# Kernel tuning notes

Measured on AMD Instinct MI355X. Metric: run time of the kernel, lower is better.

Reference implementation:

```python
import jax, jax.numpy as jnp
import numpy as np

N_NODES = 1_000_000
N_EDGES = 16_000_000


def _lin_init(key, fan_in, fan_out):
    bound = 1.0 / np.sqrt(fan_in)
    kw, kb = jax.random.split(key)
    W = jax.random.uniform(kw, (fan_in, fan_out), jnp.float32, -bound, bound)
    b = jax.random.uniform(kb, (fan_out,), jnp.float32, -bound, bound)
    return W, b


def setup_inputs() -> dict:
    key = jax.random.key(0)
    ks = jax.random.split(key, 7)
    x = jax.random.normal(ks[0], (N_NODES, 2), jnp.float32)
    edge_index = jax.random.randint(ks[1], (2, N_EDGES), 0, N_NODES, dtype=jnp.int32)
    W1, b1 = _lin_init(ks[2], 2, 4)
    W2, b2 = _lin_init(ks[3], 4, 3)
    W3, b3 = _lin_init(ks[4], 3, 4)
    W4, b4 = _lin_init(ks[5], 4, 3)
    W5, b5 = _lin_init(ks[6], 3, 1)
    return {"x": x, "edge_index": edge_index,
            "W1": W1, "b1": b1, "W2": W2, "b2": b2,
            "W3": W3, "b3": b3, "W4": W4, "b4": b4,
            "W5": W5, "b5": b5}


def gcn_conv(x, W, b, src, dst, n):
    """PyG GCNConv: add self-loops, symmetric D^-1/2 (A+I) D^-1/2 normalization."""
    h = x @ W                                   # [n, out] transform first (tiny GEMM)
    loop = jnp.arange(n, dtype=src.dtype)
    s = jnp.concatenate([src, loop])            # sources incl. self loops
    d = jnp.concatenate([dst, loop])            # targets incl. self loops
    deg = jax.ops.segment_sum(jnp.ones(s.shape, h.dtype), d, num_segments=n)
    dinv = jnp.where(deg > 0, jax.lax.rsqrt(deg), 0.0)
    norm = dinv[s] * dinv[d]                    # [E+n]
    out = jax.ops.segment_sum(h[s] * norm[:, None], d, num_segments=n)
    return out + b


def reference(x, edge_index, W1, b1, W2, b2, W3, b3, W4, b4, W5, b5):
    n = x.shape[0]
    src, dst = edge_index[0], edge_index[1]
    h = jax.nn.relu(gcn_conv(x, W1, b1, src, dst, n))
    h = jax.nn.sigmoid(gcn_conv(h, W2, b2, src, dst, n))
    # saveLaplacianError only stores a scalar side-effect (self.llLoss); it does
    # not affect the returned output, so it is omitted.
    h = jax.nn.relu(h @ W3 + b3)
    h = jax.nn.relu(h @ W4 + b4)
    out = h @ W5 + b5                           # [n, 1]
    return jnp.squeeze(out, axis=-1)
```

## Files before the change

kernel.cpp:

```cpp
#include <hip/hip_runtime.h>
#include <hip/hip_bf16.h>
#include <hip/hip_fp16.h>


constexpr int NT = 256;
constexpr int SCAN_E = 1024;
constexpr int B2 = 11;
constexpr int BN = 1 << B2;
constexpr int NBMAX = 512;
constexpr int NBIN = 1024;
constexpr int TILE = 8192;
constexpr int AT = 1024;
constexpr int SENT = (int)0x80000000;

typedef int   v4i __attribute__((ext_vector_type(4)));
typedef float v2f __attribute__((ext_vector_type(2)));

__device__ __forceinline__ int4 ldnt4(const int* p) {
    v4i v = __builtin_nontemporal_load((const v4i*)p);
    int4 r; r.x = v.x; r.y = v.y; r.z = v.z; r.w = v.w; return r;
}
__device__ __forceinline__ float2 ldnt2f(const float* p) {
    v2f v = __builtin_nontemporal_load((const v2f*)p);
    return make_float2(v.x, v.y);
}
__device__ __forceinline__ float2 h2f2(unsigned u) {
    __half2 h = __builtin_bit_cast(__half2, u);
    return __half22float2(h);
}
__device__ __forceinline__ unsigned f2h2(float a, float b) {
    return __builtin_bit_cast(unsigned, __floats2half2_rn(a, b));
}
__device__ __forceinline__ void pk_add_lds(unsigned* p, unsigned v) {
    asm volatile("ds_pk_add_f16 %0, %1"
                 :: "v"((unsigned)(size_t)p), "v"(v) : "memory");
}

__global__ void k_binhist(const int* __restrict__ src, const int* __restrict__ dst,
                          int* __restrict__ ghist, int E, int halfN) {
    __shared__ int cnt[NBIN];
    int t0 = blockIdx.x * TILE;
    for (int l = threadIdx.x; l < NBIN; l += NT) cnt[l] = 0;
    __syncthreads();
    for (int k = 0; k < TILE / (NT * 4); ++k) {
        int idx = t0 + (k * NT + threadIdx.x) * 4;
        if (idx + 3 < E) {
            int4 d4 = ldnt4(dst + idx);
            int4 s4 = ldnt4(src + idx);
            atomicAdd(&cnt[((d4.x >> B2) << 1) | (s4.x >= halfN)], 1);
            atomicAdd(&cnt[((d4.y >> B2) << 1) | (s4.y >= halfN)], 1);
            atomicAdd(&cnt[((d4.z >> B2) << 1) | (s4.z >= halfN)], 1);
            atomicAdd(&cnt[((d4.w >> B2) << 1) | (s4.w >= halfN)], 1);
        } else {
            for (int j = 0; j < 4; ++j)
                if (idx + j < E) {
                    int s = src[idx + j], d = dst[idx + j];
                    atomicAdd(&cnt[((d >> B2) << 1) | (s >= halfN)], 1);
                }
        }
    }
    __syncthreads();
    for (int l = threadIdx.x; l < NBIN; l += NT)
        if (cnt[l]) atomicAdd(&ghist[l], cnt[l]);
}

__global__ void k_scanbuckets(const int* __restrict__ ghist, int* __restrict__ gbase,
                              int* __restrict__ gcur) {
    __shared__ int part[NBIN];
    int tid = threadIdx.x;
    int t = ghist[tid];
    int p = (t + 3) & ~3;
    part[tid] = p;
    __syncthreads();
    for (int off = 1; off < NBIN; off <<= 1) {
        int v = (tid >= off) ? part[tid - off] : 0;
        __syncthreads();
        part[tid] += v;
        __syncthreads();
    }
    int excl = part[tid] - p;
    gbase[tid] = excl; gcur[tid] = excl;
    if (tid == NBIN - 1) gbase[NBIN] = part[NBIN - 1];
}

__global__ void k_pad(const int* __restrict__ ghist, const int* __restrict__ gbase,
                      int* __restrict__ pairs) {
    int b = threadIdx.x;
    int e = gbase[b] + ghist[b];
    int nxt = gbase[b + 1];
    for (; e < nxt; ++e) pairs[e] = SENT;
}

__global__ void __launch_bounds__(512)
k_binscatter(const int* __restrict__ src, const int* __restrict__ dst,
             int* __restrict__ gcur, int* __restrict__ pairs,
             int E, int halfN) {
    __shared__ int cnt[NBIN], cur[NBIN], gpos[NBIN];
    __shared__ int lbase2[NBIN + 1];
    __shared__ int part[512];
    __shared__ int lbuf[TILE];
    __shared__ int totalSh;
    int t0 = blockIdx.x * TILE;
    int tid = threadIdx.x;
    cnt[2 * tid] = 0; cnt[2 * tid + 1] = 0;
    __syncthreads();
    for (int k = 0; k < TILE / (512 * 4); ++k) {
        int idx = t0 + (k * 512 + tid) * 4;
        if (idx + 3 < E) {
            int4 d4 = ldnt4(dst + idx);
            int4 s4 = ldnt4(src + idx);
            atomicAdd(&cnt[((d4.x >> B2) << 1) | (s4.x >= halfN)], 1);
            atomicAdd(&cnt[((d4.y >> B2) << 1) | (s4.y >= halfN)], 1);
            atomicAdd(&cnt[((d4.z >> B2) << 1) | (s4.z >= halfN)], 1);
            atomicAdd(&cnt[((d4.w >> B2) << 1) | (s4.w >= halfN)], 1);
        } else {
            for (int j = 0; j < 4; ++j)
                if (idx + j < E) {
                    int s = src[idx + j], d = dst[idx + j];
                    atomicAdd(&cnt[((d >> B2) << 1) | (s >= halfN)], 1);
                }
        }
    }
    __syncthreads();
    int c0 = cnt[2 * tid], c1 = cnt[2 * tid + 1];
    int t = c0 + c1;
    part[tid] = t;
    __syncthreads();
    for (int off = 1; off < 512; off <<= 1) {
        int v = (tid >= off) ? part[tid - off] : 0;
        __syncthreads();
        part[tid] += v;
        __syncthreads();
    }
    int ex = part[tid] - t;
    lbase2[2 * tid] = ex;          cur[2 * tid] = ex;
    lbase2[2 * tid + 1] = ex + c0; cur[2 * tid + 1] = ex + c0;
    if (tid == 511) { lbase2[NBIN] = part[511]; totalSh = part[511]; }
    if (c0) gpos[2 * tid]     = atomicAdd(&gcur[2 * tid], c0);
    if (c1) gpos[2 * tid + 1] = atomicAdd(&gcur[2 * tid + 1], c1);
    __syncthreads();
    for (int k = 0; k < TILE / (512 * 4); ++k) {
        int idx = t0 + (k * 512 + tid) * 4;
        if (idx + 3 < E) {
            int4 s4 = ldnt4(src + idx);
            int4 d4 = ldnt4(dst + idx);
            int b, sl;
            b = ((d4.x >> B2) << 1) | (s4.x >= halfN); sl = atomicAdd(&cur[b], 1);
            lbuf[sl] = s4.x | ((d4.x & (BN - 1)) << 20);
            b = ((d4.y >> B2) << 1) | (s4.y >= halfN); sl = atomicAdd(&cur[b], 1);
            lbuf[sl] = s4.y | ((d4.y & (BN - 1)) << 20);
            b = ((d4.z >> B2) << 1) | (s4.z >= halfN); sl = atomicAdd(&cur[b], 1);
            lbuf[sl] = s4.z | ((d4.z & (BN - 1)) << 20);
            b = ((d4.w >> B2) << 1) | (s4.w >= halfN); sl = atomicAdd(&cur[b], 1);
            lbuf[sl] = s4.w | ((d4.w & (BN - 1)) << 20);
        } else {
            for (int j = 0; j < 4; ++j) {
                if (idx + j < E) {
                    int s = src[idx + j], d = dst[idx + j];
                    int b = ((d >> B2) << 1) | (s >= halfN);
                    int sl = atomicAdd(&cur[b], 1);
                    lbuf[sl] = s | ((d & (BN - 1)) << 20);
                }
            }
        }
    }
    __syncthreads();
    int total = totalSh;
    for (int idx = tid; idx < total; idx += 512) {
        int lo = 0, hi = NBIN - 1;
        while (lo < hi) {
            int mid = (lo + hi + 1) >> 1;
            if (lbase2[mid] <= idx) lo = mid; else hi = mid - 1;
        }
        pairs[gpos[lo] + (idx - lbase2[lo])] = lbuf[idx];
    }
}

__global__ void __launch_bounds__(AT)
k_prep(const int* __restrict__ pairs, const int* __restrict__ gbase,
       const float2* __restrict__ x,
       float* __restrict__ dinv, unsigned* __restrict__ y16, int N) {
    __shared__ int cnt[BN];
    int b = blockIdx.x, tid = threadIdx.x;
    int eBeg = gbase[2 * b], eEnd = gbase[2 * b + 2];
    for (int l = tid; l < BN; l += AT) cnt[l] = 0;
    __syncthreads();
    for (int idx = eBeg + (tid << 2); idx < eEnd; idx += AT * 4) {
        int4 v4 = ldnt4(pairs + idx);
        atomicAdd(&cnt[(((unsigned)v4.x) >> 20) & (BN - 1)], (v4.x >= 0) ? 1 : 0);
        atomicAdd(&cnt[(((unsigned)v4.y) >> 20) & (BN - 1)], (v4.y >= 0) ? 1 : 0);
        atomicAdd(&cnt[(((unsigned)v4.z) >> 20) & (BN - 1)], (v4.z >= 0) ? 1 : 0);
        atomicAdd(&cnt[(((unsigned)v4.w) >> 20) & (BN - 1)], (v4.w >= 0) ? 1 : 0);
    }
    __syncthreads();
    int base = b << B2;
    for (int j = tid; j < BN; j += AT) {
        int i = base + j;
        if (i < N) {
            float di = rsqrtf((float)(cnt[j] + 1));
            dinv[i] = di;
            float2 xi = ldnt2f((const float*)(x + i));
            y16[i] = f2h2(xi.x * di, xi.y * di);
        }
    }
}

__global__ void __launch_bounds__(AT)
k_bagg1(const int* __restrict__ pairs, const int* __restrict__ gbase,
        const unsigned* __restrict__ y16, const float2* __restrict__ x,
        const float* __restrict__ dinv,
        const float* __restrict__ W1, const float* __restrict__ b1,
        const float* __restrict__ W2,
        float2* __restrict__ partA, float* __restrict__ partB,
        uint2* __restrict__ hfull, int N) {
    __shared__ unsigned accH[BN];
    int b = blockIdx.x, tid = threadIdx.x;
    int eBeg = gbase[2 * b], eEnd = gbase[2 * b + 2];
    for (int l = tid; l < BN; l += AT) accH[l] = 0u;
    __syncthreads();
    for (int idx = eBeg + (tid << 3); idx < eEnd; idx += AT * 8) {
        int4 a = ldnt4(pairs + idx);
        int idx2 = idx + 4;
        int4 bb;
        if (idx2 < eEnd) bb = ldnt4(pairs + idx2);
        else { bb.x = SENT; bb.y = SENT; bb.z = SENT; bb.w = SENT; }
        int sv[8] = {a.x, a.y, a.z, a.w, bb.x, bb.y, bb.z, bb.w};
        unsigned rv[8];
        #pragma unroll
        for (int q = 0; q < 8; ++q)
            rv[q] = y16[sv[q] & 0xFFFFF];
        #pragma unroll
        for (int q = 0; q < 8; ++q) {
            unsigned data = (sv[q] >= 0) ? rv[q] : 0u;
            int dl = (((unsigned)sv[q]) >> 20) & (BN - 1);
            pk_add_lds(&accH[dl], data);
        }
    }
    __syncthreads();
    int base = b << B2;
    for (int j = tid; j < BN; j += AT) {
        int i = base + j;
        if (i >= N) continue;
        float2 a = h2f2(accH[j]);
        float di = dinv[i];
        float2 xi = ldnt2f((const float*)(x + i));
        float ay0 = a.x + xi.x * di;
        float ay1 = a.y + xi.y * di;
        float o0 = fmaxf(di * (ay0 * W1[0] + ay1 * W1[4]) + b1[0], 0.f);
        float o1 = fmaxf(di * (ay0 * W1[1] + ay1 * W1[5]) + b1[1], 0.f);
        float o2 = fmaxf(di * (ay0 * W1[2] + ay1 * W1[6]) + b1[2], 0.f);
        float o3 = fmaxf(di * (ay0 * W1[3] + ay1 * W1[7]) + b1[3], 0.f);
        float h0 = (o0 * W2[0] + o1 * W2[3] + o2 * W2[6] + o3 * W2[9])  * di;
        float h1 = (o0 * W2[1] + o1 * W2[4] + o2 * W2[7] + o3 * W2[10]) * di;
        float hv2 = (o0 * W2[2] + o1 * W2[5] + o2 * W2[8] + o3 * W2[11]) * di;
        v2f sA; sA.x = h0; sA.y = h1;
        __builtin_nontemporal_store(sA, (v2f*)(partA + i));
        __builtin_nontemporal_store(hv2, partB + i);
        uint2 hp; hp.x = f2h2(h0, h1); hp.y = f2h2(hv2, 0.f);
        hfull[i] = hp;
    }
}

__global__ void __launch_bounds__(AT)
k_bagg2lo(const int* __restrict__ pairs, const int* __restrict__ gbase,
          const uint2* __restrict__ hfull,
          float2* __restrict__ partA, float* __restrict__ partB, int N) {
    __shared__ unsigned acc01[BN];
    __shared__ float acc2[BN];
    int b = blockIdx.x, tid = threadIdx.x;
    int eBeg = gbase[2 * b], eEnd = gbase[2 * b + 1];
    for (int l = tid; l < BN; l += AT) { acc01[l] = 0u; acc2[l] = 0.f; }
    __syncthreads();
    for (int idx = eBeg + (tid << 3); idx < eEnd; idx += AT * 8) {
        int4 a = ldnt4(pairs + idx);
        int idx2 = idx + 4;
        int4 bb;
        if (idx2 < eEnd) bb = ldnt4(pairs + idx2);
        else { bb.x = SENT; bb.y = SENT; bb.z = SENT; bb.w = SENT; }
        int sv[8] = {a.x, a.y, a.z, a.w, bb.x, bb.y, bb.z, bb.w};
        uint2 r[8];
        #pragma unroll
        for (int q = 0; q < 8; ++q)
            r[q] = hfull[sv[q] & 0xFFFFF];
        #pragma unroll
        for (int q = 0; q < 8; ++q) {
            int dl = (((unsigned)sv[q]) >> 20) & (BN - 1);
            unsigned d01 = (sv[q] >= 0) ? r[q].x : 0u;
            float    f2v = (sv[q] >= 0) ? h2f2(r[q].y).x : 0.f;
            pk_add_lds(&acc01[dl], d01);
            atomicAdd(&acc2[dl], f2v);
        }
    }
    __syncthreads();
    int base = b << B2;
    for (int j = tid; j < BN; j += AT) {
        int i = base + j;
        if (i >= N) continue;
        float2 a01 = h2f2(acc01[j]);
        float2 pa = ldnt2f((const float*)(partA + i));
        float pb = __builtin_nontemporal_load(partB + i);
        v2f oA; oA.x = pa.x + a01.x; oA.y = pa.y + a01.y;
        __builtin_nontemporal_store(oA, (v2f*)(partA + i));
        __builtin_nontemporal_store(pb + acc2[j], partB + i);
    }
}

__global__ void __launch_bounds__(AT)
k_bagg2hi(const int* __restrict__ pairs, const int* __restrict__ gbase,
          const uint2* __restrict__ hfull,
          const float2* __restrict__ partA, const float* __restrict__ partB,
          const float* __restrict__ dinv,
          const float* __restrict__ b2,
          const float* __restrict__ W3, const float* __restrict__ b3,
          const float* __restrict__ W4, const float* __restrict__ b4,
          const float* __restrict__ W5, const float* __restrict__ b5,
          float* __restrict__ out, int N) {
    __shared__ unsigned acc01[BN];
    __shared__ float acc2[BN];
    int b = blockIdx.x, tid = threadIdx.x;
    int eBeg = gbase[2 * b + 1], eEnd = gbase[2 * b + 2];
    for (int l = tid; l < BN; l += AT) { acc01[l] = 0u; acc2[l] = 0.f; }
    __syncthreads();
    for (int idx = eBeg + (tid << 3); idx < eEnd; idx += AT * 8) {
        int4 a = ldnt4(pairs + idx);
        int idx2 = idx + 4;
        int4 bb;
        if (idx2 < eEnd) bb = ldnt4(pairs + idx2);
        else { bb.x = SENT; bb.y = SENT; bb.z = SENT; bb.w = SENT; }
        int sv[8] = {a.x, a.y, a.z, a.w, bb.x, bb.y, bb.z, bb.w};
        uint2 r[8];
        #pragma unroll
        for (int q = 0; q < 8; ++q)
            r[q] = hfull[sv[q] & 0xFFFFF];
        #pragma unroll
        for (int q = 0; q < 8; ++q) {
            int dl = (((unsigned)sv[q]) >> 20) & (BN - 1);
            unsigned d01 = (sv[q] >= 0) ? r[q].x : 0u;
            float    f2v = (sv[q] >= 0) ? h2f2(r[q].y).x : 0.f;
            pk_add_lds(&acc01[dl], d01);
            atomicAdd(&acc2[dl], f2v);
        }
    }
    __syncthreads();
    int base = b << B2;
    for (int j = tid; j < BN; j += AT) {
        int i = base + j;
        if (i >= N) continue;
        float2 a01 = h2f2(acc01[j]);
        float2 pa = ldnt2f((const float*)(partA + i));
        float pb = __builtin_nontemporal_load(partB + i);
        float s0 = pa.x + a01.x;
        float s1 = pa.y + a01.y;
        float s2 = pb + acc2[j];
        float di = __builtin_nontemporal_load(dinv + i);
        float z0 = di * s0 + b2[0];
        float z1 = di * s1 + b2[1];
        float z2 = di * s2 + b2[2];
        float g0 = 1.f / (1.f + expf(-z0));
        float g1 = 1.f / (1.f + expf(-z1));
        float g2 = 1.f / (1.f + expf(-z2));
        float t0 = fmaxf(g0 * W3[0] + g1 * W3[4] + g2 * W3[8]  + b3[0], 0.f);
        float t1 = fmaxf(g0 * W3[1] + g1 * W3[5] + g2 * W3[9]  + b3[1], 0.f);
        float t2 = fmaxf(g0 * W3[2] + g1 * W3[6] + g2 * W3[10] + b3[2], 0.f);
        float t3 = fmaxf(g0 * W3[3] + g1 * W3[7] + g2 * W3[11] + b3[3], 0.f);
        float u0 = fmaxf(t0 * W4[0] + t1 * W4[3] + t2 * W4[6] + t3 * W4[9]  + b4[0], 0.f);
        float u1 = fmaxf(t0 * W4[1] + t1 * W4[4] + t2 * W4[7] + t3 * W4[10] + b4[1], 0.f);
        float u2 = fmaxf(t0 * W4[2] + t1 * W4[5] + t2 * W4[8] + t3 * W4[11] + b4[2], 0.f);
        out[i] = u0 * W5[0] + u1 * W5[1] + u2 * W5[2] + b5[0];
    }
}

__global__ void k_deg(const int* __restrict__ dst, int* __restrict__ deg, int E) {
    int e = blockIdx.x * blockDim.x + threadIdx.x;
    if (e < E) atomicAdd(deg + dst[e], 1);
}
__global__ void k_scan1(const int* __restrict__ deg, int* __restrict__ row,
                        int* __restrict__ bsum, int N) {
    __shared__ int lds[NT];
    int base = blockIdx.x * SCAN_E + threadIdx.x * 4;
    int d0 = 0, d1 = 0, d2 = 0, d3 = 0;
    if (base + 3 < N) {
        int4 v = *(const int4*)(deg + base);
        d0 = v.x; d1 = v.y; d2 = v.z; d3 = v.w;
    } else {
        if (base     < N) d0 = deg[base];
        if (base + 1 < N) d1 = deg[base + 1];
        if (base + 2 < N) d2 = deg[base + 2];
        if (base + 3 < N) d3 = deg[base + 3];
    }
    int t = d0 + d1 + d2 + d3;
    lds[threadIdx.x] = t;
    __syncthreads();
    for (int off = 1; off < NT; off <<= 1) {
        int v = (threadIdx.x >= off) ? lds[threadIdx.x - off] : 0;
        __syncthreads();
        lds[threadIdx.x] += v;
        __syncthreads();
    }
    int excl = lds[threadIdx.x] - t;
    if (threadIdx.x == NT - 1) bsum[blockIdx.x] = lds[NT - 1];
    if (base     < N) row[base]     = excl;
    if (base + 1 < N) row[base + 1] = excl + d0;
    if (base + 2 < N) row[base + 2] = excl + d0 + d1;
    if (base + 3 < N) row[base + 3] = excl + d0 + d1 + d2;
}
__global__ void k_scan2(int* __restrict__ bsum, int M) {
    __shared__ int lds[NT];
    int base = threadIdx.x * 4;
    int d0 = 0, d1 = 0, d2 = 0, d3 = 0;
    if (base     < M) d0 = bsum[base];
    if (base + 1 < M) d1 = bsum[base + 1];
    if (base + 2 < M) d2 = bsum[base + 2];
    if (base + 3 < M) d3 = bsum[base + 3];
    int t = d0 + d1 + d2 + d3;
    lds[threadIdx.x] = t;
    __syncthreads();
    for (int off = 1; off < NT; off <<= 1) {
        int v = (threadIdx.x >= off) ? lds[threadIdx.x - off] : 0;
        __syncthreads();
        lds[threadIdx.x] += v;
        __syncthreads();
    }
    int excl = lds[threadIdx.x] - t;
    if (base     < M) bsum[base]     = excl;
    if (base + 1 < M) bsum[base + 1] = excl + d0;
    if (base + 2 < M) bsum[base + 2] = excl + d0 + d1;
    if (base + 3 < M) bsum[base + 3] = excl + d0 + d1 + d2;
}
__global__ void k_scan3(int* __restrict__ row, const int* __restrict__ bsum, int N) {
    int base = blockIdx.x * SCAN_E + threadIdx.x * 4;
    int add = bsum[blockIdx.x];
    if (base + 3 < N) {
        int4 v = *(int4*)(row + base);
        v.x += add; v.y += add; v.z += add; v.w += add;
        *(int4*)(row + base) = v;
    } else {
        if (base     < N) row[base]     += add;
        if (base + 1 < N) row[base + 1] += add;
        if (base + 2 < N) row[base + 2] += add;
    }
}
__global__ void k_scatter(const int* __restrict__ src, const int* __restrict__ dst,
                          int* __restrict__ row, int* __restrict__ ss, int E) {
    int e = blockIdx.x * blockDim.x + threadIdx.x;
    if (e >= E) return;
    int s = src[e], d = dst[e];
    int slot = atomicAdd(row + d, 1);
    ss[slot] = s;
}
__global__ void k_node1_fb(const float2* __restrict__ x, const int* __restrict__ deg,
                           const float* __restrict__ W1,
                           float* __restrict__ dinv, float4* __restrict__ hp, int N) {
    int i = blockIdx.x * blockDim.x + threadIdx.x;
    if (i >= N) return;
    float2 xi = x[i];
    float di = rsqrtf((float)(deg[i] + 1));
    dinv[i] = di;
    float4 h;
    h.x = (xi.x * W1[0] + xi.y * W1[4]) * di;
    h.y = (xi.x * W1[1] + xi.y * W1[5]) * di;
    h.z = (xi.x * W1[2] + xi.y * W1[6]) * di;
    h.w = (xi.x * W1[3] + xi.y * W1[7]) * di;
    hp[i] = h;
}
__global__ void k_aggf1_fb(const int* __restrict__ row, const int* __restrict__ ss,
                           const float4* __restrict__ hp1, const float* __restrict__ dinv,
                           const float* __restrict__ b1, const float* __restrict__ W2,
                           float4* __restrict__ hp2, int N) {
    int i = blockIdx.x * blockDim.x + threadIdx.x;
    if (i >= N) return;
    int beg = (i == 0) ? 0 : row[i - 1];
    int end = row[i];
    float4 a = hp1[i];
    for (int e = beg; e < end; ++e) {
        float4 ha = hp1[ss[e]];
        a.x += ha.x; a.y += ha.y; a.z += ha.z; a.w += ha.w;
    }
    float di = dinv[i];
    float o0 = fmaxf(di * a.x + b1[0], 0.f);
    float o1 = fmaxf(di * a.y + b1[1], 0.f);
    float o2 = fmaxf(di * a.z + b1[2], 0.f);
    float o3 = fmaxf(di * a.w + b1[3], 0.f);
    float4 h;
    h.x = (o0 * W2[0] + o1 * W2[3] + o2 * W2[6] + o3 * W2[9])  * di;
    h.y = (o0 * W2[1] + o1 * W2[4] + o2 * W2[7] + o3 * W2[10]) * di;
    h.z = (o0 * W2[2] + o1 * W2[5] + o2 * W2[8] + o3 * W2[11]) * di;
    h.w = 0.f;
    hp2[i] = h;
}
__global__ void k_aggf2_fb(const int* __restrict__ row, const int* __restrict__ ss,
                           const float4* __restrict__ hp2, const float* __restrict__ dinv,
                           const float* __restrict__ b2,
                           const float* __restrict__ W3, const float* __restrict__ b3,
                           const float* __restrict__ W4, const float* __restrict__ b4,
                           const float* __restrict__ W5, const float* __restrict__ b5,
                           float* __restrict__ out, int N) {
    int i = blockIdx.x * blockDim.x + threadIdx.x;
    if (i >= N) return;
    int beg = (i == 0) ? 0 : row[i - 1];
    int end = row[i];
    float4 a = hp2[i];
    for (int e = beg; e < end; ++e) {
        float4 ha = hp2[ss[e]];
        a.x += ha.x; a.y += ha.y; a.z += ha.z;
    }
    float di = dinv[i];
    float z0 = di * a.x + b2[0];
    float z1 = di * a.y + b2[1];
    float z2 = di * a.z + b2[2];
    float g0 = 1.f / (1.f + expf(-z0));
    float g1 = 1.f / (1.f + expf(-z1));
    float g2 = 1.f / (1.f + expf(-z2));
    float t0 = fmaxf(g0 * W3[0] + g1 * W3[4] + g2 * W3[8]  + b3[0], 0.f);
    float t1 = fmaxf(g0 * W3[1] + g1 * W3[5] + g2 * W3[9]  + b3[1], 0.f);
    float t2 = fmaxf(g0 * W3[2] + g1 * W3[6] + g2 * W3[10] + b3[2], 0.f);
    float t3 = fmaxf(g0 * W3[3] + g1 * W3[7] + g2 * W3[11] + b3[3], 0.f);
    float u0 = fmaxf(t0 * W4[0] + t1 * W4[3] + t2 * W4[6] + t3 * W4[9]  + b4[0], 0.f);
    float u1 = fmaxf(t0 * W4[1] + t1 * W4[4] + t2 * W4[7] + t3 * W4[10] + b4[1], 0.f);
    float u2 = fmaxf(t0 * W4[2] + t1 * W4[5] + t2 * W4[8] + t3 * W4[11] + b4[2], 0.f);
    out[i] = u0 * W5[0] + u1 * W5[1] + u2 * W5[2] + b5[0];
}

extern "C" void kernel_launch(void* const* d_in, const int* in_sizes, int n_in,
                              void* d_out, int out_size, void* d_ws, size_t ws_size,
                              hipStream_t stream) {
    const float* x  = (const float*)d_in[0];
    const int*   ei = (const int*)d_in[1];
    const float* W1 = (const float*)d_in[2];
    const float* b1 = (const float*)d_in[3];
    const float* W2 = (const float*)d_in[4];
    const float* b2 = (const float*)d_in[5];
    const float* W3 = (const float*)d_in[6];
    const float* b3 = (const float*)d_in[7];
    const float* W4 = (const float*)d_in[8];
    const float* b4 = (const float*)d_in[9];
    const float* W5 = (const float*)d_in[10];
    const float* b5 = (const float*)d_in[11];

    const int N = in_sizes[0] / 2;
    const int E = in_sizes[1] / 2;
    const int* src = ei;
    const int* dst = ei + E;

    const int gbN = (N + NT - 1) / NT;
    const int gbE = (E + NT - 1) / NT;
    const int tiles = (E + TILE - 1) / TILE;
    const int NB = (N + BN - 1) >> B2;
    const int halfN = (N + 1) >> 1;

    char* ws = (char*)d_ws;

    size_t szPairs  = (size_t)(E + 4 * NBIN) * 4;
    size_t offPartA = (szPairs + 15) & ~(size_t)15;
    size_t offPartB = offPartA + (size_t)N * 8;
    size_t offY16   = offPartB + (size_t)N * 4;
    size_t offDinv  = offY16 + (size_t)N * 4;
    size_t offHfull = offDinv + (size_t)N * 4;
    size_t offHist  = (offHfull + (size_t)N * 8 + 15) & ~(size_t)15;
    size_t need1    = offHist + 3 * (NBIN + 1) * 4 + 64;

    if (N <= (1 << 20) && NB <= NBMAX && ws_size >= need1) {
        int*      pairs = (int*)ws;
        float2*   partA = (float2*)(ws + offPartA);
        float*    partB = (float*)(ws + offPartB);
        unsigned* y16   = (unsigned*)(ws + offY16);
        float*    dinv  = (float*)(ws + offDinv);
        uint2*    hfull = (uint2*)(ws + offHfull);
        int*      ghist = (int*)(ws + offHist);
        int*      gbase = ghist + (NBIN + 1);
        int*      gcur  = gbase + (NBIN + 1);

        hipMemsetAsync(ghist, 0, (NBIN + 1) * 4, stream);
        k_binhist    <<<tiles, NT, 0, stream>>>(src, dst, ghist, E, halfN);
        k_scanbuckets<<<1, NBIN, 0, stream>>>(ghist, gbase, gcur);
        k_pad        <<<1, NBIN, 0, stream>>>(ghist, gbase, pairs);
        k_binscatter <<<tiles, 512, 0, stream>>>(src, dst, gcur, pairs, E, halfN);
        k_prep       <<<NB, AT, 0, stream>>>(pairs, gbase, (const float2*)x,
                                             dinv, y16, N);
        k_bagg1      <<<NB, AT, 0, stream>>>(pairs, gbase, y16, (const float2*)x,
                                             dinv, W1, b1, W2, partA, partB,
                                             hfull, N);
        k_bagg2lo    <<<NB, AT, 0, stream>>>(pairs, gbase, hfull, partA, partB, N);
        k_bagg2hi    <<<NB, AT, 0, stream>>>(pairs, gbase, hfull, partA, partB,
                                             dinv, b2, W3, b3, W4, b4, W5, b5,
                                             (float*)d_out, N);
        return;
    }

    const int nScanBlocks = (N + SCAN_E - 1) / SCAN_E;
    size_t need2 = (size_t)N * 44 + (size_t)E * 4 + (size_t)nScanBlocks * 4 + 256;
    if (ws_size >= need2 && nScanBlocks <= NT * 4) {
        float4* hp1  = (float4*)ws;
        float4* hp2  = (float4*)(ws + (size_t)N * 16);
        int*    ss   = (int*)   (ws + (size_t)N * 32);
        int*    deg  = (int*)   (ws + (size_t)N * 32 + (size_t)E * 4);
        int*    row  = (int*)   (ws + (size_t)N * 36 + (size_t)E * 4);
        float*  dinv = (float*) (ws + (size_t)N * 40 + (size_t)E * 4);
        int*    bsum = (int*)   (ws + (size_t)N * 44 + (size_t)E * 4);

        hipMemsetAsync(deg, 0, (size_t)N * 4, stream);
        k_deg     <<<gbE, NT, 0, stream>>>(dst, deg, E);
        k_scan1   <<<nScanBlocks, NT, 0, stream>>>(deg, row, bsum, N);
        k_scan2   <<<1, NT, 0, stream>>>(bsum, nScanBlocks);
        k_scan3   <<<nScanBlocks, NT, 0, stream>>>(row, bsum, N);
        k_node1_fb<<<gbN, NT, 0, stream>>>((const float2*)x, deg, W1, dinv, hp1, N);
        k_scatter <<<gbE, NT, 0, stream>>>(src, dst, row, ss, E);
        k_aggf1_fb<<<gbN, NT, 0, stream>>>(row, ss, hp1, dinv, b1, W2, hp2, N);
        k_aggf2_fb<<<gbN, NT, 0, stream>>>(row, ss, hp2, dinv, b2, W3, b3, W4, b4,
                                           W5, b5, (float*)d_out, N);
    }
}
```

Before: 696.4 us.

## Precompute per-tile bin counts and fold degree counting into the count pass

The count kernel now writes a per-tile, per-bin count matrix, which is scanned per bin, and also accumulates node degrees with global atomics. The placement kernel reads its offsets from that matrix instead of recounting the tile and taking global atomic cursors. This makes the placement deterministic and drops its counting pass. The separate prep pass that re-read pairs to count degrees becomes a simple per-node kernel. In exchange it adds 16M global atomics on the degree array, a memset of N ints, and a 1024-block scan over the count matrix.

```diff
diff --git a/kernel.cpp b/kernel.cpp
--- a/kernel.cpp
+++ b/kernel.cpp
@@ -36,8 +36,9 @@
                  :: "v"((unsigned)(size_t)p), "v"(v) : "memory");
 }
 
-__global__ void k_binhist(const int* __restrict__ src, const int* __restrict__ dst,
-                          int* __restrict__ ghist, int E, int halfN) {
+__global__ void k_count(const int* __restrict__ src, const int* __restrict__ dst,
+                        int* __restrict__ cntmat, int* __restrict__ deg,
+                        int E, int halfN, int tiles) {
     __shared__ int cnt[NBIN];
     int t0 = blockIdx.x * TILE;
     for (int l = threadIdx.x; l < NBIN; l += NT) cnt[l] = 0;
@@ -51,21 +52,52 @@
             atomicAdd(&cnt[((d4.y >> B2) << 1) | (s4.y >= halfN)], 1);
             atomicAdd(&cnt[((d4.z >> B2) << 1) | (s4.z >= halfN)], 1);
             atomicAdd(&cnt[((d4.w >> B2) << 1) | (s4.w >= halfN)], 1);
+            atomicAdd(&deg[d4.x], 1);
+            atomicAdd(&deg[d4.y], 1);
+            atomicAdd(&deg[d4.z], 1);
+            atomicAdd(&deg[d4.w], 1);
         } else {
             for (int j = 0; j < 4; ++j)
                 if (idx + j < E) {
                     int s = src[idx + j], d = dst[idx + j];
                     atomicAdd(&cnt[((d >> B2) << 1) | (s >= halfN)], 1);
+                    atomicAdd(&deg[d], 1);
                 }
         }
     }
     __syncthreads();
     for (int l = threadIdx.x; l < NBIN; l += NT)
-        if (cnt[l]) atomicAdd(&ghist[l], cnt[l]);
-}
-
-__global__ void k_scanbuckets(const int* __restrict__ ghist, int* __restrict__ gbase,
-                              int* __restrict__ gcur) {
+        cntmat[l * tiles + blockIdx.x] = cnt[l];
+}
+
+__global__ void __launch_bounds__(256)
+k_scanA(int* __restrict__ cntmat, int* __restrict__ ghist, int tiles) {
+    __shared__ int lds[256];
+    int bin = blockIdx.x;
+    int* row = cntmat + (size_t)bin * tiles;
+    int tid = threadIdx.x;
+    int carry = 0;
+    for (int base = 0; base < tiles; base += 256) {
+        int i = base + tid;
+        int v = (i < tiles) ? row[i] : 0;
+        lds[tid] = v;
+        __syncthreads();
+        for (int off = 1; off < 256; off <<= 1) {
+            int t = (tid >= off) ? lds[tid - off] : 0;
+            __syncthreads();
+            lds[tid] += t;
+            __syncthreads();
+        }
+        int incl = lds[tid];
+        int tot = lds[255];
+        if (i < tiles) row[i] = carry + incl - v;
+        carry += tot;
+        __syncthreads();
+    }
+    if (tid == 0) ghist[bin] = carry;
+}
+
+__global__ void k_scanB(const int* __restrict__ ghist, int* __restrict__ gbase) {
     __shared__ int part[NBIN];
     int tid = threadIdx.x;
     int t = ghist[tid];
@@ -78,8 +110,7 @@
         part[tid] += v;
         __syncthreads();
     }
-    int excl = part[tid] - p;
-    gbase[tid] = excl; gcur[tid] = excl;
+    gbase[tid] = part[tid] - p;
     if (tid == NBIN - 1) gbase[NBIN] = part[NBIN - 1];
 }
 
@@ -92,37 +123,26 @@
 }
 
 __global__ void __launch_bounds__(512)
-k_binscatter(const int* __restrict__ src, const int* __restrict__ dst,
-             int* __restrict__ gcur, int* __restrict__ pairs,
-             int E, int halfN) {
-    __shared__ int cnt[NBIN], cur[NBIN], gpos[NBIN];
+k_place(const int* __restrict__ src, const int* __restrict__ dst,
+        const int* __restrict__ cntmat, const int* __restrict__ ghist,
+        const int* __restrict__ gbase, int* __restrict__ pairs,
+        int E, int halfN, int tiles) {
+    __shared__ int cur[NBIN], gposc[NBIN];
     __shared__ int lbase2[NBIN + 1];
     __shared__ int part[512];
     __shared__ int lbuf[TILE];
     __shared__ int totalSh;
-    int t0 = blockIdx.x * TILE;
+    int tile = blockIdx.x;
+    int t0 = tile * TILE;
     int tid = threadIdx.x;
-    cnt[2 * tid] = 0; cnt[2 * tid + 1] = 0;
-    __syncthreads();
-    for (int k = 0; k < TILE / (512 * 4); ++k) {
-        int idx = t0 + (k * 512 + tid) * 4;
-        if (idx + 3 < E) {
-            int4 d4 = ldnt4(dst + idx);
-            int4 s4 = ldnt4(src + idx);
-            atomicAdd(&cnt[((d4.x >> B2) << 1) | (s4.x >= halfN)], 1);
-            atomicAdd(&cnt[((d4.y >> B2) << 1) | (s4.y >= halfN)], 1);
-            atomicAdd(&cnt[((d4.z >> B2) << 1) | (s4.z >= halfN)], 1);
-            atomicAdd(&cnt[((d4.w >> B2) << 1) | (s4.w >= halfN)], 1);
-        } else {
-            for (int j = 0; j < 4; ++j)
-                if (idx + j < E) {
-                    int s = src[idx + j], d = dst[idx + j];
-                    atomicAdd(&cnt[((d >> B2) << 1) | (s >= halfN)], 1);
-                }
-        }
-    }
-    __syncthreads();
-    int c0 = cnt[2 * tid], c1 = cnt[2 * tid + 1];
+    int bA = 2 * tid, bB = 2 * tid + 1;
+    int p00 = cntmat[(size_t)bA * tiles + tile];
+    int p01 = (tile + 1 < tiles) ? cntmat[(size_t)bA * tiles + tile + 1] : ghist[bA];
+    int p10 = cntmat[(size_t)bB * tiles + tile];
+    int p11 = (tile + 1 < tiles) ? cntmat[(size_t)bB * tiles + tile + 1] : ghist[bB];
+    int c0 = p01 - p00, c1 = p11 - p10;
+    gposc[bA] = gbase[bA] + p00;
+    gposc[bB] = gbase[bB] + p10;
     int t = c0 + c1;
     part[tid] = t;
     __syncthreads();
@@ -133,11 +153,9 @@
         __syncthreads();
     }
     int ex = part[tid] - t;
-    lbase2[2 * tid] = ex;          cur[2 * tid] = ex;
-    lbase2[2 * tid + 1] = ex + c0; cur[2 * tid + 1] = ex + c0;
+    lbase2[bA] = ex;      cur[bA] = ex;
+    lbase2[bB] = ex + c0; cur[bB] = ex + c0;
     if (tid == 511) { lbase2[NBIN] = part[511]; totalSh = part[511]; }
-    if (c0) gpos[2 * tid]     = atomicAdd(&gcur[2 * tid], c0);
-    if (c1) gpos[2 * tid + 1] = atomicAdd(&gcur[2 * tid + 1], c1);
     __syncthreads();
     for (int k = 0; k < TILE / (512 * 4); ++k) {
         int idx = t0 + (k * 512 + tid) * 4;
@@ -172,37 +190,18 @@
             int mid = (lo + hi + 1) >> 1;
             if (lbase2[mid] <= idx) lo = mid; else hi = mid - 1;
         }
-        pairs[gpos[lo] + (idx - lbase2[lo])] = lbuf[idx];
-    }
-}
-
-__global__ void __launch_bounds__(AT)
-k_prep(const int* __restrict__ pairs, const int* __restrict__ gbase,
-       const float2* __restrict__ x,
-       float* __restrict__ dinv, unsigned* __restrict__ y16, int N) {
-    __shared__ int cnt[BN];
-    int b = blockIdx.x, tid = threadIdx.x;
-    int eBeg = gbase[2 * b], eEnd = gbase[2 * b + 2];
-    for (int l = tid; l < BN; l += AT) cnt[l] = 0;
-    __syncthreads();
-    for (int idx = eBeg + (tid << 2); idx < eEnd; idx += AT * 4) {
-        int4 v4 = ldnt4(pairs + idx);
-        atomicAdd(&cnt[(((unsigned)v4.x) >> 20) & (BN - 1)], (v4.x >= 0) ? 1 : 0);
-        atomicAdd(&cnt[(((unsigned)v4.y) >> 20) & (BN - 1)], (v4.y >= 0) ? 1 : 0);
-        atomicAdd(&cnt[(((unsigned)v4.z) >> 20) & (BN - 1)], (v4.z >= 0) ? 1 : 0);
-        atomicAdd(&cnt[(((unsigned)v4.w) >> 20) & (BN - 1)], (v4.w >= 0) ? 1 : 0);
-    }
-    __syncthreads();
-    int base = b << B2;
-    for (int j = tid; j < BN; j += AT) {
-        int i = base + j;
-        if (i < N) {
-            float di = rsqrtf((float)(cnt[j] + 1));
-            dinv[i] = di;
-            float2 xi = ldnt2f((const float*)(x + i));
-            y16[i] = f2h2(xi.x * di, xi.y * di);
-        }
-    }
+        pairs[gposc[lo] + (idx - lbase2[lo])] = lbuf[idx];
+    }
+}
+
+__global__ void k_prepy(const int* __restrict__ deg, const float2* __restrict__ x,
+                        float* __restrict__ dinv, unsigned* __restrict__ y16, int N) {
+    int i = blockIdx.x * blockDim.x + threadIdx.x;
+    if (i >= N) return;
+    float di = rsqrtf((float)(deg[i] + 1));
+    dinv[i] = di;
+    float2 xi = ldnt2f((const float*)(x + i));
+    y16[i] = f2h2(xi.x * di, xi.y * di);
 }
 
 __global__ void __launch_bounds__(AT)
@@ -556,34 +555,38 @@
     size_t offY16   = offPartB + (size_t)N * 4;
     size_t offDinv  = offY16 + (size_t)N * 4;
     size_t offHfull = offDinv + (size_t)N * 4;
-    size_t offHist  = (offHfull + (size_t)N * 8 + 15) & ~(size_t)15;
-    size_t need1    = offHist + 3 * (NBIN + 1) * 4 + 64;
+    size_t offCnt   = (offHfull + (size_t)N * 8 + 15) & ~(size_t)15;
+    size_t offHist  = (offCnt + (size_t)NBIN * tiles * 4 + 15) & ~(size_t)15;
+    size_t need1    = offHist + (size_t)(2 * NBIN + 2) * 4 + 64;
 
     if (N <= (1 << 20) && NB <= NBMAX && ws_size >= need1) {
-        int*      pairs = (int*)ws;
-        float2*   partA = (float2*)(ws + offPartA);
-        float*    partB = (float*)(ws + offPartB);
-        unsigned* y16   = (unsigned*)(ws + offY16);
-        float*    dinv  = (float*)(ws + offDinv);
-        uint2*    hfull = (uint2*)(ws + offHfull);
-        int*      ghist = (int*)(ws + offHist);
-        int*      gbase = ghist + (NBIN + 1);
-        int*      gcur  = gbase + (NBIN + 1);
-
-        hipMemsetAsync(ghist, 0, (NBIN + 1) * 4, stream);
-        k_binhist    <<<tiles, NT, 0, stream>>>(src, dst, ghist, E, halfN);
-        k_scanbuckets<<<1, NBIN, 0, stream>>>(ghist, gbase, gcur);
-        k_pad        <<<1, NBIN, 0, stream>>>(ghist, gbase, pairs);
-        k_binscatter <<<tiles, 512, 0, stream>>>(src, dst, gcur, pairs, E, halfN);
-        k_prep       <<<NB, AT, 0, stream>>>(pairs, gbase, (const float2*)x,
-                                             dinv, y16, N);
-        k_bagg1      <<<NB, AT, 0, stream>>>(pairs, gbase, y16, (const float2*)x,
-                                             dinv, W1, b1, W2, partA, partB,
-                                             hfull, N);
-        k_bagg2lo    <<<NB, AT, 0, stream>>>(pairs, gbase, hfull, partA, partB, N);
-        k_bagg2hi    <<<NB, AT, 0, stream>>>(pairs, gbase, hfull, partA, partB,
-                                             dinv, b2, W3, b3, W4, b4, W5, b5,
-                                             (float*)d_out, N);
+        int*      pairs  = (int*)ws;
+        float2*   partA  = (float2*)(ws + offPartA);
+        float*    partB  = (float*)(ws + offPartB);
+        int*      deg    = (int*)(ws + offPartB);
+        unsigned* y16    = (unsigned*)(ws + offY16);
+        float*    dinv   = (float*)(ws + offDinv);
+        uint2*    hfull  = (uint2*)(ws + offHfull);
+        int*      cntmat = (int*)(ws + offCnt);
+        int*      ghist  = (int*)(ws + offHist);
+        int*      gbase  = ghist + NBIN;
+
+        hipMemsetAsync(deg, 0, (size_t)N * 4, stream);
+        k_count  <<<tiles, NT, 0, stream>>>(src, dst, cntmat, deg, E, halfN, tiles);
+        k_scanA  <<<NBIN, 256, 0, stream>>>(cntmat, ghist, tiles);
+        k_scanB  <<<1, NBIN, 0, stream>>>(ghist, gbase);
+        k_pad    <<<1, NBIN, 0, stream>>>(ghist, gbase, pairs);
+        k_place  <<<tiles, 512, 0, stream>>>(src, dst, cntmat, ghist, gbase,
+                                             pairs, E, halfN, tiles);
+        k_prepy  <<<(N + 255) / 256, 256, 0, stream>>>(deg, (const float2*)x,
+                                                       dinv, y16, N);
+        k_bagg1  <<<NB, AT, 0, stream>>>(pairs, gbase, y16, (const float2*)x,
+                                         dinv, W1, b1, W2, partA, partB,
+                                         hfull, N);
+        k_bagg2lo<<<NB, AT, 0, stream>>>(pairs, gbase, hfull, partA, partB, N);
+        k_bagg2hi<<<NB, AT, 0, stream>>>(pairs, gbase, hfull, partA, partB,
+                                         dinv, b2, W3, b3, W4, b4, W5, b5,
+                                         (float*)d_out, N);
         return;
     }
 
```

After: 1.184 ms. 70.0% more time.
